# Kernel optimization log

Hardware: AMD Instinct MI355X
Metric: run time of the kernel (lower is better)

The kernel has to match this reference:

```python
import jax, jax.numpy as jnp
import numpy as np

B, S, C = 2, 4096, 512
H = 8            # num heads
D = C // H       # head dim = 64


def setup_inputs() -> dict:
    key = jax.random.key(0)
    ks = jax.random.split(key, 5)
    s = 0.02
    return {
        "hidden_states": jax.random.normal(ks[0], (B, S, C), dtype=jnp.float32),
        "Wq": jax.random.normal(ks[1], (C, C), dtype=jnp.float32) * s,
        "Wk": jax.random.normal(ks[2], (C, C), dtype=jnp.float32) * s,
        "Wv": jax.random.normal(ks[3], (C, C), dtype=jnp.float32) * s,
        "Wo": jax.random.normal(ks[4], (C, C), dtype=jnp.float32) * s,
        "bo": jnp.zeros((C,), dtype=jnp.float32),
    }


def reference(hidden_states, Wq, Wk, Wv, Wo, bo):
    # Self-attention path of AttnProcessor (encoder_hidden_states=None,
    # no norms, no mask, residual_connection=False, rescale=1.0).
    b, s, c = hidden_states.shape
    scale = jnp.float32(D) ** -0.5
    # QKV projections (Linear, no bias as in diffusers defaults)
    q = hidden_states @ Wq.T   # [b,s,c]
    k = hidden_states @ Wk.T
    v = hidden_states @ Wv.T
    # head_to_batch_dim: [b,s,c] -> [b,s,h,d]
    q = q.reshape(b, s, H, D)
    k = k.reshape(b, s, H, D)
    v = v.reshape(b, s, H, D)
    # get_attention_scores: scaled QK^T + softmax (full O(S^2) matrix, as in source)
    scores = jnp.einsum("bqhd,bkhd->bhqk", q, k) * scale   # [b,h,s,s]
    probs = jax.nn.softmax(scores, axis=-1)
    # bmm with V, batch_to_head_dim
    out = jnp.einsum("bhqk,bkhd->bqhd", probs, v).reshape(b, s, c)
    # to_out[0] (Linear with bias); to_out[1] is Dropout (identity at eval)
    out = out @ Wo.T + bo
    return out
```

## Files before the change

kernel.cpp:

```cpp
#include <hip/hip_runtime.h>
#include <hip/hip_bf16.h>

#define BB 2
#define SS 4096
#define CC 512
#define HH 8
#define DD 64
#define MM (BB*SS)

typedef __bf16 bf16;
typedef __attribute__((ext_vector_type(8))) __bf16 bf16x8;
typedef __attribute__((ext_vector_type(4))) __bf16 bf16x4;
typedef __attribute__((ext_vector_type(4))) float f32x4;

#define LP 72
#define QSCALE 0.18033688f

__device__ __forceinline__ float exp2_fast(float x) {
  float r;
  asm("v_exp_f32 %0, %1" : "=v"(r) : "v"(x));
  return r;
}

__device__ __forceinline__ bf16x8 cvt8(const float4 a, const float4 b) {
  bf16x8 r;
  r[0]=(bf16)a.x; r[1]=(bf16)a.y; r[2]=(bf16)a.z; r[3]=(bf16)a.w;
  r[4]=(bf16)b.x; r[5]=(bf16)b.y; r[6]=(bf16)b.z; r[7]=(bf16)b.w;
  return r;
}

__global__ __launch_bounds__(256) void cvt_f32_bf16(
    const float* __restrict__ src, bf16* __restrict__ dst)
{
  size_t e = ((size_t)blockIdx.x * 256 + threadIdx.x) * 8;
  float4 a = ((const float4*)(src + e))[0];
  float4 b = ((const float4*)(src + e))[1];
  *(bf16x8*)(dst + e) = cvt8(a, b);
}

__global__ __launch_bounds__(256) void cvt_w(
    const float* __restrict__ Wq, const float* __restrict__ Wk,
    const float* __restrict__ Wv, bf16* __restrict__ Wb)
{
  size_t e = ((size_t)blockIdx.x * 256 + threadIdx.x) * 8;
  const int tens = (int)(e >> 18);
  const float* src = ((tens == 0) ? Wq : (tens == 1) ? Wk : Wv) + (e & 262143);
  const float sc = (tens == 0) ? QSCALE : 1.f;
  float4 a = ((const float4*)src)[0];
  float4 b = ((const float4*)src)[1];
  bf16x8 r;
  r[0]=(bf16)(a.x*sc); r[1]=(bf16)(a.y*sc); r[2]=(bf16)(a.z*sc); r[3]=(bf16)(a.w*sc);
  r[4]=(bf16)(b.x*sc); r[5]=(bf16)(b.y*sc); r[6]=(bf16)(b.z*sc); r[7]=(bf16)(b.w*sc);
  *(bf16x8*)(Wb + e) = r;
}

__global__ __launch_bounds__(256) void qkv_gemm(
    const bf16* __restrict__ Xb, const bf16* __restrict__ Wb,
    bf16* __restrict__ qp, bf16* __restrict__ kp, bf16* __restrict__ vtp)
{
  __shared__ bf16 Aa[64*LP];
  __shared__ bf16 Ab[64*LP];
  __shared__ bf16 Ba[64*LP];
  __shared__ bf16 Bb[64*LP];
  const int m0  = blockIdx.x * 128;
  const int nf0 = blockIdx.y * 128;
  const int tens = nf0 >> 9;
  const int n0 = nf0 & 511;

  const int t = threadIdx.x;
  const int w = t >> 6;
  const int lane = t & 63;
  const int l15 = lane & 15;
  const int quad = lane >> 4;
  const int srow = t >> 2;
  const int scol = (t & 3) << 4;

  f32x4 acc[2][2][4];
  #pragma unroll
  for (int mi = 0; mi < 2; ++mi)
    #pragma unroll
    for (int ni = 0; ni < 2; ++ni)
      #pragma unroll
      for (int nt = 0; nt < 4; ++nt)
        #pragma unroll
        for (int r = 0; r < 4; ++r) acc[mi][ni][nt][r] = 0.f;

  for (int k0 = 0; k0 < CC; k0 += 64) {
    __syncthreads();
    {
      const bf16* sa = Xb + (size_t)(m0 + srow) * CC + k0 + scol;
      *(bf16x8*)&Aa[srow*LP + scol]     = ((const bf16x8*)sa)[0];
      *(bf16x8*)&Aa[srow*LP + scol + 8] = ((const bf16x8*)sa)[1];
      const bf16* sb = Xb + (size_t)(m0 + 64 + srow) * CC + k0 + scol;
      *(bf16x8*)&Ab[srow*LP + scol]     = ((const bf16x8*)sb)[0];
      *(bf16x8*)&Ab[srow*LP + scol + 8] = ((const bf16x8*)sb)[1];
      const bf16* s1 = Wb + (size_t)(nf0 + srow) * CC + k0 + scol;
      *(bf16x8*)&Ba[srow*LP + scol]     = ((const bf16x8*)s1)[0];
      *(bf16x8*)&Ba[srow*LP + scol + 8] = ((const bf16x8*)s1)[1];
      const bf16* s2 = Wb + (size_t)(nf0 + 64 + srow) * CC + k0 + scol;
      *(bf16x8*)&Bb[srow*LP + scol]     = ((const bf16x8*)s2)[0];
      *(bf16x8*)&Bb[srow*LP + scol + 8] = ((const bf16x8*)s2)[1];
    }
    __syncthreads();
    #pragma unroll
    for (int c = 0; c < 2; ++c) {
      bf16x8 afa = *(const bf16x8*)&Aa[(w*16 + l15)*LP + c*32 + quad*8];
      bf16x8 afb = *(const bf16x8*)&Ab[(w*16 + l15)*LP + c*32 + quad*8];
      #pragma unroll
      for (int nt = 0; nt < 4; ++nt) {
        bf16x8 ba = *(const bf16x8*)&Ba[(nt*16 + l15)*LP + c*32 + quad*8];
        bf16x8 bb = *(const bf16x8*)&Bb[(nt*16 + l15)*LP + c*32 + quad*8];
        acc[0][0][nt] = __builtin_amdgcn_mfma_f32_16x16x32_bf16(afa, ba, acc[0][0][nt], 0, 0, 0);
        acc[1][0][nt] = __builtin_amdgcn_mfma_f32_16x16x32_bf16(afb, ba, acc[1][0][nt], 0, 0, 0);
        acc[0][1][nt] = __builtin_amdgcn_mfma_f32_16x16x32_bf16(afa, bb, acc[0][1][nt], 0, 0, 0);
        acc[1][1][nt] = __builtin_amdgcn_mfma_f32_16x16x32_bf16(afb, bb, acc[1][1][nt], 0, 0, 0);
      }
    }
  }

  bf16* plane = (tens == 0) ? qp : ((tens == 1) ? kp : vtp);
  const int c8 = (t & 7) * 8;

  auto epi = [&](const f32x4* as, int mt0, int nb) {
    const int b = mt0 >> 12, s0g = mt0 & 4095;
    const int h = nb >> 6;
    __syncthreads();
    if (tens < 2) {
      #pragma unroll
      for (int nt = 0; nt < 4; ++nt)
        #pragma unroll
        for (int r = 0; r < 4; ++r)
          Aa[(w*16 + quad*4 + r)*LP + nt*16 + l15] = (bf16)as[nt][r];
    } else {
      #pragma unroll
      for (int nt = 0; nt < 4; ++nt)
        #pragma unroll
        for (int r = 0; r < 4; ++r)
          Aa[(nt*16 + l15)*LP + w*16 + quad*4 + r] = (bf16)as[nt][r];
    }
    __syncthreads();
    #pragma unroll
    for (int i = 0; i < 2; ++i) {
      const int row = (t >> 3) + 32*i;
      bf16x8 v = *(const bf16x8*)&Aa[row*LP + c8];
      if (tens < 2) {
        *(bf16x8*)&plane[((size_t)((b*HH + h)*SS) + s0g + row)*DD + c8] = v;
      } else {
        *(bf16x8*)&plane[((size_t)((b*HH + h)*DD) + row)*SS + s0g + c8] = v;
      }
    }
  };

  epi(acc[0][0], m0,      n0);
  epi(acc[1][0], m0 + 64, n0);
  epi(acc[0][1], m0,      n0 + 64);
  epi(acc[1][1], m0 + 64, n0 + 64);
}

__global__ __launch_bounds__(256) void attn_fa(
    const bf16* __restrict__ qpl, const bf16* __restrict__ kpl,
    const bf16* __restrict__ vtpl, bf16* __restrict__ aout)
{
  __shared__ bf16 Kt[2][64*LP];
  __shared__ bf16 Vt[2][64*LP];

  const int t = threadIdx.x;
  const int w = t >> 6;
  const int lane = t & 63;
  const int l15 = lane & 15;
  const int quad = lane >> 4;

  const int bh = blockIdx.y;
  const int q0 = blockIdx.x * 128;
  const size_t plane = (size_t)SS * DD;
  const bf16* Qp = qpl + (size_t)bh * plane;
  const bf16* Kp = kpl + (size_t)bh * plane;
  const bf16* Vg = vtpl + (size_t)bh * plane;

  bf16x8 qf[2][2];
  #pragma unroll
  for (int wq = 0; wq < 2; ++wq) {
    const bf16* qr = Qp + (size_t)(q0 + w*32 + wq*16 + l15) * DD + quad*8;
    qf[wq][0] = *(const bf16x8*)qr;
    qf[wq][1] = *(const bf16x8*)(qr + 32);
  }

  f32x4 o[2][4];
  float rs[2] = {0.f, 0.f};
  #pragma unroll
  for (int wq = 0; wq < 2; ++wq)
    #pragma unroll
    for (int nt = 0; nt < 4; ++nt)
      #pragma unroll
      for (int r = 0; r < 4; ++r) o[wq][nt][r] = 0.f;

  const int r0 = t >> 3;
  const int c0 = (t & 7) * 8;
  const int koff = (c0 >> 5)*32 + ((c0 >> 3) & 3)*4;

  bf16x8 ka0, ka1;
  bf16x4 v00, v01, v10, v11;
  {
    ka0 = *(const bf16x8*)&Kp[(size_t)r0*DD + c0];
    ka1 = *(const bf16x8*)&Kp[(size_t)(r0 + 32)*DD + c0];
    v00 = *(const bf16x4*)&Vg[(size_t)r0*SS + koff];
    v01 = *(const bf16x4*)&Vg[(size_t)r0*SS + koff + 16];
    v10 = *(const bf16x4*)&Vg[(size_t)(r0+32)*SS + koff];
    v11 = *(const bf16x4*)&Vg[(size_t)(r0+32)*SS + koff + 16];
    *(bf16x8*)&Kt[0][r0*LP + c0]      = ka0;
    *(bf16x8*)&Kt[0][(r0+32)*LP + c0] = ka1;
    bf16x8 vv;
    vv[0]=v00[0]; vv[1]=v00[1]; vv[2]=v00[2]; vv[3]=v00[3];
    vv[4]=v01[0]; vv[5]=v01[1]; vv[6]=v01[2]; vv[7]=v01[3];
    *(bf16x8*)&Vt[0][r0*LP + c0] = vv;
    vv[0]=v10[0]; vv[1]=v10[1]; vv[2]=v10[2]; vv[3]=v10[3];
    vv[4]=v11[0]; vv[5]=v11[1]; vv[6]=v11[2]; vv[7]=v11[3];
    *(bf16x8*)&Vt[0][(r0+32)*LP + c0] = vv;
  }
  __syncthreads();

  for (int it = 0; it < SS/64; ++it) {
    const int cur = it & 1;
    if (it < SS/64 - 1) {
      const int kb = (it + 1) * 64;
      ka0 = *(const bf16x8*)&Kp[(size_t)(kb + r0)*DD + c0];
      ka1 = *(const bf16x8*)&Kp[(size_t)(kb + r0 + 32)*DD + c0];
      v00 = *(const bf16x4*)&Vg[(size_t)r0*SS + kb + koff];
      v01 = *(const bf16x4*)&Vg[(size_t)r0*SS + kb + koff + 16];
      v10 = *(const bf16x4*)&Vg[(size_t)(r0+32)*SS + kb + koff];
      v11 = *(const bf16x4*)&Vg[(size_t)(r0+32)*SS + kb + koff + 16];
    }

    f32x4 st[2][4];
    #pragma unroll
    for (int nt = 0; nt < 4; ++nt) {
      bf16x8 kf0 = *(const bf16x8*)&Kt[cur][(nt*16 + l15)*LP + quad*8];
      bf16x8 kf1 = *(const bf16x8*)&Kt[cur][(nt*16 + l15)*LP + 32 + quad*8];
      #pragma unroll
      for (int wq = 0; wq < 2; ++wq) {
        f32x4 z; z[0]=z[1]=z[2]=z[3]=0.f;
        z = __builtin_amdgcn_mfma_f32_16x16x32_bf16(kf0, qf[wq][0], z, 0, 0, 0);
        z = __builtin_amdgcn_mfma_f32_16x16x32_bf16(kf1, qf[wq][1], z, 0, 0, 0);
        st[wq][nt] = z;
      }
    }

    bf16x8 pb[2][2];
    #pragma unroll
    for (int wq = 0; wq < 2; ++wq) {
      float acc_s = 0.f;
      #pragma unroll
      for (int nt = 0; nt < 4; ++nt)
        #pragma unroll
        for (int r = 0; r < 4; ++r) {
          float pv = exp2_fast(st[wq][nt][r]);
          acc_s += pv;
          pb[wq][nt >> 1][(nt & 1)*4 + r] = (bf16)pv;
        }
      rs[wq] += acc_s;
    }

    #pragma unroll
    for (int kbh = 0; kbh < 2; ++kbh) {
      #pragma unroll
      for (int nt = 0; nt < 4; ++nt) {
        bf16x8 vf = *(const bf16x8*)&Vt[cur][(nt*16 + l15)*LP + kbh*32 + quad*8];
        #pragma unroll
        for (int wq = 0; wq < 2; ++wq)
          o[wq][nt] = __builtin_amdgcn_mfma_f32_16x16x32_bf16(vf, pb[wq][kbh], o[wq][nt], 0, 0, 0);
      }
    }

    if (it < SS/64 - 1) {
      const int nxt = cur ^ 1;
      *(bf16x8*)&Kt[nxt][r0*LP + c0]      = ka0;
      *(bf16x8*)&Kt[nxt][(r0+32)*LP + c0] = ka1;
      bf16x8 vv;
      vv[0]=v00[0]; vv[1]=v00[1]; vv[2]=v00[2]; vv[3]=v00[3];
      vv[4]=v01[0]; vv[5]=v01[1]; vv[6]=v01[2]; vv[7]=v01[3];
      *(bf16x8*)&Vt[nxt][r0*LP + c0] = vv;
      vv[0]=v10[0]; vv[1]=v10[1]; vv[2]=v10[2]; vv[3]=v10[3];
      vv[4]=v11[0]; vv[5]=v11[1]; vv[6]=v11[2]; vv[7]=v11[3];
      *(bf16x8*)&Vt[nxt][(r0+32)*LP + c0] = vv;
      __syncthreads();
    }
  }

  const int b = bh >> 3, h = bh & 7;
  #pragma unroll
  for (int wq = 0; wq < 2; ++wq) {
    float s = rs[wq];
    s += __shfl_xor(s, 16);
    s += __shfl_xor(s, 32);
    const float inv = 1.f / s;
    const size_t row = (size_t)(b*SS + q0 + w*32 + wq*16 + l15) * CC + h*DD;
    #pragma unroll
    for (int nt = 0; nt < 4; ++nt) {
      bf16x4 ov;
      #pragma unroll
      for (int r = 0; r < 4; ++r) ov[r] = (bf16)(o[wq][nt][r] * inv);
      *(bf16x4*)&aout[row + nt*16 + quad*4] = ov;
    }
  }
}

__global__ __launch_bounds__(256) void out_gemm(
    const bf16* __restrict__ A, const bf16* __restrict__ Wob,
    const float* __restrict__ bo, float* __restrict__ out)
{
  __shared__ bf16 Aa[64*LP];
  __shared__ bf16 Ab[64*LP];
  __shared__ bf16 Bt[64*LP];
  const int m0 = blockIdx.x * 128;
  const int n0 = blockIdx.y * 64;

  const int t = threadIdx.x;
  const int w = t >> 6;
  const int lane = t & 63;
  const int l15 = lane & 15;
  const int quad = lane >> 4;
  const int srow = t >> 2;
  const int scol = (t & 3) << 4;

  f32x4 aca[4], acb[4];
  #pragma unroll
  for (int i = 0; i < 4; ++i)
    #pragma unroll
    for (int j = 0; j < 4; ++j) { aca[i][j] = 0.f; acb[i][j] = 0.f; }

  for (int k0 = 0; k0 < CC; k0 += 64) {
    __syncthreads();
    {
      const bf16* sa = A + (size_t)(m0 + srow) * CC + k0 + scol;
      *(bf16x8*)&Aa[srow*LP + scol]     = ((const bf16x8*)sa)[0];
      *(bf16x8*)&Aa[srow*LP + scol + 8] = ((const bf16x8*)sa)[1];
      const bf16* sb = A + (size_t)(m0 + 64 + srow) * CC + k0 + scol;
      *(bf16x8*)&Ab[srow*LP + scol]     = ((const bf16x8*)sb)[0];
      *(bf16x8*)&Ab[srow*LP + scol + 8] = ((const bf16x8*)sb)[1];
      const bf16* s1 = Wob + (size_t)(n0 + srow) * CC + k0 + scol;
      *(bf16x8*)&Bt[srow*LP + scol]     = ((const bf16x8*)s1)[0];
      *(bf16x8*)&Bt[srow*LP + scol + 8] = ((const bf16x8*)s1)[1];
    }
    __syncthreads();
    #pragma unroll
    for (int c = 0; c < 2; ++c) {
      bf16x8 afa = *(const bf16x8*)&Aa[(w*16 + l15)*LP + c*32 + quad*8];
      bf16x8 afb = *(const bf16x8*)&Ab[(w*16 + l15)*LP + c*32 + quad*8];
      #pragma unroll
      for (int nt = 0; nt < 4; ++nt) {
        bf16x8 bfr = *(const bf16x8*)&Bt[(nt*16 + l15)*LP + c*32 + quad*8];
        aca[nt] = __builtin_amdgcn_mfma_f32_16x16x32_bf16(afa, bfr, aca[nt], 0, 0, 0);
        acb[nt] = __builtin_amdgcn_mfma_f32_16x16x32_bf16(afb, bfr, acb[nt], 0, 0, 0);
      }
    }
  }

  #pragma unroll
  for (int nt = 0; nt < 4; ++nt) {
    const int ng = n0 + nt*16 + l15;
    const float bias = bo[ng];
    #pragma unroll
    for (int r = 0; r < 4; ++r) {
      const int mga = m0 + w*16 + quad*4 + r;
      out[(size_t)mga*CC + ng] = aca[nt][r] + bias;
      const int mgb = m0 + 64 + w*16 + quad*4 + r;
      out[(size_t)mgb*CC + ng] = acb[nt][r] + bias;
    }
  }
}

extern "C" void kernel_launch(void* const* d_in, const int* in_sizes, int n_in,
                              void* d_out, int out_size, void* d_ws, size_t ws_size,
                              hipStream_t stream) {
  const float* hs = (const float*)d_in[0];
  const float* Wq = (const float*)d_in[1];
  const float* Wk = (const float*)d_in[2];
  const float* Wv = (const float*)d_in[3];
  const float* Wo = (const float*)d_in[4];
  const float* bo = (const float*)d_in[5];
  float* out = (float*)d_out;

  const size_t PE = (size_t)BB*HH*SS*DD;
  bf16* ws   = (bf16*)d_ws;
  bf16* qp   = ws;
  bf16* kp   = ws + PE;
  bf16* vtp  = ws + 2*PE;
  bf16* Xb   = ws + 3*PE;
  bf16* aout = ws + 3*PE;
  bf16* Wob  = qp;
  bf16* Wb   = ws + 4*PE;

  cvt_f32_bf16<<<dim3(2048),      256, 0, stream>>>(hs, Xb);
  cvt_w       <<<dim3(384),       256, 0, stream>>>(Wq, Wk, Wv, Wb);
  qkv_gemm<<<dim3(MM/128, 12),    256, 0, stream>>>(Xb, Wb, qp, kp, vtp);
  attn_fa <<<dim3(SS/128, BB*HH), 256, 0, stream>>>(qp, kp, vtp, aout);
  cvt_f32_bf16<<<dim3(128),       256, 0, stream>>>(Wo, Wob);
  out_gemm<<<dim3(MM/128, CC/64), 256, 0, stream>>>(aout, Wob, bo, out);
}
```

Baseline: 200.5 us.

## Compute softmax row sums via MFMA with ones and widen out-GEMM N tile

In the attention kernel, the per-thread scalar accumulation of exp values and the final cross-lane shuffle reduction are replaced by an extra MFMA against a vector of ones, so the row sum comes out of the matrix unit already reduced. This takes VALU adds out of the hot loop but adds two MFMAs per kbh step and sums the bf16-rounded probabilities instead of the fp32 values. In the output GEMM, the N tile grows from 64 to 128, giving each A tile twice the reuse and halving the grid, at the cost of more accumulator registers and fewer blocks.

```diff
diff --git a/kernel.cpp b/kernel.cpp
--- a/kernel.cpp
+++ b/kernel.cpp
@@ -185,14 +185,20 @@
     qf[wq][1] = *(const bf16x8*)(qr + 32);
   }
 
-  f32x4 o[2][4];
-  float rs[2] = {0.f, 0.f};
-  #pragma unroll
-  for (int wq = 0; wq < 2; ++wq)
+  bf16x8 ones;
+  #pragma unroll
+  for (int j = 0; j < 8; ++j) ones[j] = (bf16)1.0f;
+
+  f32x4 o[2][4], la[2];
+  #pragma unroll
+  for (int wq = 0; wq < 2; ++wq) {
+    #pragma unroll
+    for (int r = 0; r < 4; ++r) la[wq][r] = 0.f;
     #pragma unroll
     for (int nt = 0; nt < 4; ++nt)
       #pragma unroll
       for (int r = 0; r < 4; ++r) o[wq][nt][r] = 0.f;
+  }
 
   const int r0 = t >> 3;
   const int c0 = (t & 7) * 8;
@@ -247,18 +253,12 @@
 
     bf16x8 pb[2][2];
     #pragma unroll
-    for (int wq = 0; wq < 2; ++wq) {
-      float acc_s = 0.f;
+    for (int wq = 0; wq < 2; ++wq)
       #pragma unroll
       for (int nt = 0; nt < 4; ++nt)
         #pragma unroll
-        for (int r = 0; r < 4; ++r) {
-          float pv = exp2_fast(st[wq][nt][r]);
-          acc_s += pv;
-          pb[wq][nt >> 1][(nt & 1)*4 + r] = (bf16)pv;
-        }
-      rs[wq] += acc_s;
-    }
+        for (int r = 0; r < 4; ++r)
+          pb[wq][nt >> 1][(nt & 1)*4 + r] = (bf16)exp2_fast(st[wq][nt][r]);
 
     #pragma unroll
     for (int kbh = 0; kbh < 2; ++kbh) {
@@ -269,6 +269,9 @@
         for (int wq = 0; wq < 2; ++wq)
           o[wq][nt] = __builtin_amdgcn_mfma_f32_16x16x32_bf16(vf, pb[wq][kbh], o[wq][nt], 0, 0, 0);
       }
+      #pragma unroll
+      for (int wq = 0; wq < 2; ++wq)
+        la[wq] = __builtin_amdgcn_mfma_f32_16x16x32_bf16(ones, pb[wq][kbh], la[wq], 0, 0, 0);
     }
 
     if (it < SS/64 - 1) {
@@ -289,10 +292,7 @@
   const int b = bh >> 3, h = bh & 7;
   #pragma unroll
   for (int wq = 0; wq < 2; ++wq) {
-    float s = rs[wq];
-    s += __shfl_xor(s, 16);
-    s += __shfl_xor(s, 32);
-    const float inv = 1.f / s;
+    const float inv = 1.f / la[wq][0];
     const size_t row = (size_t)(b*SS + q0 + w*32 + wq*16 + l15) * CC + h*DD;
     #pragma unroll
     for (int nt = 0; nt < 4; ++nt) {
@@ -310,9 +310,10 @@
 {
   __shared__ bf16 Aa[64*LP];
   __shared__ bf16 Ab[64*LP];
-  __shared__ bf16 Bt[64*LP];
+  __shared__ bf16 Ba[64*LP];
+  __shared__ bf16 Bb[64*LP];
   const int m0 = blockIdx.x * 128;
-  const int n0 = blockIdx.y * 64;
+  const int n0 = blockIdx.y * 128;
 
   const int t = threadIdx.x;
   const int w = t >> 6;
@@ -322,11 +323,15 @@
   const int srow = t >> 2;
   const int scol = (t & 3) << 4;
 
-  f32x4 aca[4], acb[4];
-  #pragma unroll
-  for (int i = 0; i < 4; ++i)
-    #pragma unroll
-    for (int j = 0; j < 4; ++j) { aca[i][j] = 0.f; acb[i][j] = 0.f; }
+  f32x4 acc[2][2][4];
+  #pragma unroll
+  for (int mi = 0; mi < 2; ++mi)
+    #pragma unroll
+    for (int ni = 0; ni < 2; ++ni)
+      #pragma unroll
+      for (int nt = 0; nt < 4; ++nt)
+        #pragma unroll
+        for (int r = 0; r < 4; ++r) acc[mi][ni][nt][r] = 0.f;
 
   for (int k0 = 0; k0 < CC; k0 += 64) {
     __syncthreads();
@@ -338,8 +343,11 @@
       *(bf16x8*)&Ab[srow*LP + scol]     = ((const bf16x8*)sb)[0];
       *(bf16x8*)&Ab[srow*LP + scol + 8] = ((const bf16x8*)sb)[1];
       const bf16* s1 = Wob + (size_t)(n0 + srow) * CC + k0 + scol;
-      *(bf16x8*)&Bt[srow*LP + scol]     = ((const bf16x8*)s1)[0];
-      *(bf16x8*)&Bt[srow*LP + scol + 8] = ((const bf16x8*)s1)[1];
+      *(bf16x8*)&Ba[srow*LP + scol]     = ((const bf16x8*)s1)[0];
+      *(bf16x8*)&Ba[srow*LP + scol + 8] = ((const bf16x8*)s1)[1];
+      const bf16* s2 = Wob + (size_t)(n0 + 64 + srow) * CC + k0 + scol;
+      *(bf16x8*)&Bb[srow*LP + scol]     = ((const bf16x8*)s2)[0];
+      *(bf16x8*)&Bb[srow*LP + scol + 8] = ((const bf16x8*)s2)[1];
     }
     __syncthreads();
     #pragma unroll
@@ -348,23 +356,29 @@
       bf16x8 afb = *(const bf16x8*)&Ab[(w*16 + l15)*LP + c*32 + quad*8];
       #pragma unroll
       for (int nt = 0; nt < 4; ++nt) {
-        bf16x8 bfr = *(const bf16x8*)&Bt[(nt*16 + l15)*LP + c*32 + quad*8];
-        aca[nt] = __builtin_amdgcn_mfma_f32_16x16x32_bf16(afa, bfr, aca[nt], 0, 0, 0);
-        acb[nt] = __builtin_amdgcn_mfma_f32_16x16x32_bf16(afb, bfr, acb[nt], 0, 0, 0);
-      }
-    }
-  }
-
-  #pragma unroll
-  for (int nt = 0; nt < 4; ++nt) {
-    const int ng = n0 + nt*16 + l15;
-    const float bias = bo[ng];
-    #pragma unroll
-    for (int r = 0; r < 4; ++r) {
-      const int mga = m0 + w*16 + quad*4 + r;
-      out[(size_t)mga*CC + ng] = aca[nt][r] + bias;
-      const int mgb = m0 + 64 + w*16 + quad*4 + r;
-      out[(size_t)mgb*CC + ng] = acb[nt][r] + bias;
+        bf16x8 ba = *(const bf16x8*)&Ba[(nt*16 + l15)*LP + c*32 + quad*8];
+        bf16x8 bb = *(const bf16x8*)&Bb[(nt*16 + l15)*LP + c*32 + quad*8];
+        acc[0][0][nt] = __builtin_amdgcn_mfma_f32_16x16x32_bf16(afa, ba, acc[0][0][nt], 0, 0, 0);
+        acc[1][0][nt] = __builtin_amdgcn_mfma_f32_16x16x32_bf16(afb, ba, acc[1][0][nt], 0, 0, 0);
+        acc[0][1][nt] = __builtin_amdgcn_mfma_f32_16x16x32_bf16(afa, bb, acc[0][1][nt], 0, 0, 0);
+        acc[1][1][nt] = __builtin_amdgcn_mfma_f32_16x16x32_bf16(afb, bb, acc[1][1][nt], 0, 0, 0);
+      }
+    }
+  }
+
+  #pragma unroll
+  for (int ni = 0; ni < 2; ++ni) {
+    #pragma unroll
+    for (int nt = 0; nt < 4; ++nt) {
+      const int ng = n0 + ni*64 + nt*16 + l15;
+      const float bias = bo[ng];
+      #pragma unroll
+      for (int r = 0; r < 4; ++r) {
+        const int mga = m0 + w*16 + quad*4 + r;
+        out[(size_t)mga*CC + ng] = acc[0][ni][nt][r] + bias;
+        const int mgb = m0 + 64 + w*16 + quad*4 + r;
+        out[(size_t)mgb*CC + ng] = acc[1][ni][nt][r] + bias;
+      }
     }
   }
 }
@@ -395,5 +409,5 @@
   qkv_gemm<<<dim3(MM/128, 12),    256, 0, stream>>>(Xb, Wb, qp, kp, vtp);
   attn_fa <<<dim3(SS/128, BB*HH), 256, 0, stream>>>(qp, kp, vtp, aout);
   cvt_f32_bf16<<<dim3(128),       256, 0, stream>>>(Wo, Wob);
-  out_gemm<<<dim3(MM/128, CC/64), 256, 0, stream>>>(aout, Wob, bo, out);
-}
+  out_gemm<<<dim3(MM/128, CC/128), 256, 0, stream>>>(aout, Wob, bo, out);
+}
```

Measured after the change: 205.1 us. 1.02x slower.
